# Optimization experiments

Hardware: AMD Instinct MI355X
Metric: run time of the kernel (lower is better)

## Reference

```python
import jax, jax.numpy as jnp
import numpy as np

WS, WS2, UP = 8, 16, 2
DIM, HEADS = 192, 6
HD = DIM // HEADS
SCALE = HD ** -0.5
EPS = 1e-5

def _rel_index():
    r1, c1 = np.meshgrid(np.arange(WS), np.arange(WS), indexing='ij')
    r2, c2 = np.meshgrid(np.arange(WS2), np.arange(WS2), indexing='ij')
    r1, c1 = r1.ravel(), c1.ravel()          # 64 query positions
    r2, c2 = r2.ravel(), c2.ravel()          # 256 kv positions
    rel_row = r1[:, None] - r2[None, :]
    rel_col = c1[:, None] - c2[None, :]
    off = WS * UP - 1    # 15
    span = WS + WS * UP - 1  # 23
    return jnp.asarray((rel_row + off) * span + (rel_col + off))  # (64, 256)

REL_IDX = _rel_index()

def layer_norm(x, w, b):
    m = x.mean(-1, keepdims=True)
    v = ((x - m) ** 2).mean(-1, keepdims=True)
    return (x - m) * jax.lax.rsqrt(v + EPS) * w + b

def window_partition(x, ws):
    B, H, W, C = x.shape
    x = x.reshape(B, H // ws, ws, W // ws, ws, C).transpose(0, 1, 3, 2, 4, 5)
    return x.reshape(-1, ws * ws, C)

def window_reverse(w, ws, H, W, B):
    x = w.reshape(B, H // ws, W // ws, ws, ws, -1).transpose(0, 1, 3, 2, 4, 5)
    return x.reshape(B, H, W, -1)

def setup_inputs() -> dict:
    key = jax.random.key(0)
    ks = jax.random.split(key, 8)
    B, H, W, H2, W2 = 4, 128, 128, 256, 256
    s = 0.02
    return {
        'x': jax.random.normal(ks[0], (B, H * W, DIM), jnp.float32),
        'x2': jax.random.normal(ks[1], (B, H2 * W2, DIM), jnp.float32),
        'norm1_w': jnp.ones((DIM,), jnp.float32),
        'norm1_b': jnp.zeros((DIM,), jnp.float32),
        'qkv_w': jax.random.normal(ks[2], (DIM, DIM), jnp.float32) * s,
        'qkv_b': jnp.zeros((DIM,), jnp.float32),
        'qkv2_w': jax.random.normal(ks[3], (2 * DIM, DIM), jnp.float32) * s,
        'qkv2_b': jnp.zeros((2 * DIM,), jnp.float32),
        'rel_bias': jax.random.normal(ks[4], (23 * 23, HEADS), jnp.float32) * s,
        'proj_w': jax.random.normal(ks[5], (DIM, DIM), jnp.float32) * s,
        'proj_b': jnp.zeros((DIM,), jnp.float32),
        'norm2_w': jnp.ones((DIM,), jnp.float32),
        'norm2_b': jnp.zeros((DIM,), jnp.float32),
        'fc1_w': jax.random.normal(ks[6], (4 * DIM, DIM), jnp.float32) * s,
        'fc1_b': jnp.zeros((4 * DIM,), jnp.float32),
        'fc2_w': jax.random.normal(ks[7], (DIM, 4 * DIM), jnp.float32) * s,
        'fc2_b': jnp.zeros((DIM,), jnp.float32),
        'H': 128, 'W': 128, 'H2': 256, 'W2': 256,
    }

def reference(x, x2, norm1_w, norm1_b, qkv_w, qkv_b, qkv2_w, qkv2_b, rel_bias,
              proj_w, proj_b, norm2_w, norm2_b, fc1_w, fc1_b, fc2_w, fc2_b,
              H, W, H2, W2):
    B, L, C = x.shape
    shortcut = x
    xn = layer_norm(x, norm1_w, norm1_b).reshape(B, H, W, C)
    x2r = x2.reshape(B, H2, W2, C)

    xw = window_partition(xn, WS)      # (nW, 64, C)
    x2w = window_partition(x2r, WS2)   # (nW, 256, C)

    q = (xw @ qkv_w.T + qkv_b).reshape(-1, WS * WS, HEADS, HD).transpose(0, 2, 1, 3)
    kv = (x2w @ qkv2_w.T + qkv2_b).reshape(-1, WS2 * WS2, 2, HEADS, HD).transpose(2, 0, 3, 1, 4)
    k, v = kv[0], kv[1]                # (nW, h, 256, d)

    attn = jnp.einsum('whnd,whmd->whnm', q * SCALE, k)   # (nW, h, 64, 256)
    bias = rel_bias[REL_IDX]                             # (64, 256, h)
    attn = attn + bias.transpose(2, 0, 1)[None]
    attn = jax.nn.softmax(attn, axis=-1)
    out = jnp.einsum('whnm,whmd->wnhd', attn, v).reshape(-1, WS * WS, C)
    out = out @ proj_w.T + proj_b

    x = shortcut + window_reverse(out, WS, H, W, B).reshape(B, H * W, C)
    h = layer_norm(x, norm2_w, norm2_b)
    h = jax.nn.gelu(h @ fc1_w.T + fc1_b, approximate=False)
    x = x + (h @ fc2_w.T + fc2_b)
    return x
```

## Files before the change

### kernel.cpp

```cpp
#include <hip/hip_runtime.h>
#include <hip/hip_bf16.h>
#include <math.h>

typedef unsigned int u32;
typedef unsigned short u16;

typedef __attribute__((ext_vector_type(8))) short bf16x8;
typedef __attribute__((ext_vector_type(4))) float f32x4;

__device__ __forceinline__ float bflo(u32 u){ union{u32 i; float f;} c; c.i = u << 16; return c.f; }
__device__ __forceinline__ float bfhi(u32 u){ union{u32 i; float f;} c; c.i = u & 0xffff0000u; return c.f; }
__device__ __forceinline__ float bfs(u16 s){ union{u32 i; float f;} c; c.i = ((u32)s) << 16; return c.f; }
__device__ __forceinline__ u32 packbf(float a, float b){
  union{float f; u32 i;} ca, cb; ca.f = a; cb.f = b;
  u32 ua = (ca.i + 0x7fffu + ((ca.i >> 16) & 1u)) >> 16;
  u32 ub = (cb.i + 0x7fffu + ((cb.i >> 16) & 1u)) >> 16;
  return (ua & 0xffffu) | (ub << 16);
}
__device__ __forceinline__ u16 bf1(float a){
  union{float f; u32 i;} c; c.f = a;
  return (u16)((c.i + 0x7fffu + ((c.i >> 16) & 1u)) >> 16);
}
__device__ __forceinline__ bf16x8 pack8(float f0,float f1,float f2,float f3,
                                        float f4,float f5,float f6,float f7){
  union { u32 u[4]; bf16x8 v; } cv;
  cv.u[0]=packbf(f0,f1); cv.u[1]=packbf(f2,f3); cv.u[2]=packbf(f4,f5); cv.u[3]=packbf(f6,f7);
  return cv.v;
}
__device__ __forceinline__ float gelu_exact(float v){ return 0.5f*v*(1.0f + erff(v*0.70710678118654752f)); }
__device__ __forceinline__ bool detect_f32(const u32* rawn1){ return (rawn1[0] & 0xFFFFu) == 0u; }

#define SCALE_Q 0.17677669529663687f

#define P_N1W 0
#define P_N1B 192
#define P_N2W 384
#define P_N2B 576
#define P_QKVB 768
#define P_QKV2B 960
#define P_PROJB 1344
#define P_FC1B 1536
#define P_FC2B 2304
#define P_RELB 2496
#define P_TOTAL 5670
#define W_QKV 0
#define W_QKV2 18432
#define W_PROJ 55296
#define W_FC1 73728
#define W_FC2 147456
#define W_TOTAL 221184

__device__ __forceinline__ void stage_w64x192(const u32* __restrict__ src, u32* lds, int tid){
  #pragma unroll
  for (int t = 0; t < 6; ++t) {
    int idx = tid + t*256;
    int j = idx / 24, seg = idx % 24;
    uint4 v = *(const uint4*)(src + (size_t)j*96 + seg*4);
    int byt = (j*384 + seg*16) ^ ((j&7)<<4);
    *(uint4*)((char*)lds + byt) = v;
  }
}
__device__ __forceinline__ bf16x8 lds_w64(const u32* lds, int j, int kt, int g){
  int byt = (j*384 + kt*64 + g*16) ^ ((j&7)<<4);
  return *(const bf16x8*)((const char*)lds + byt);
}
__device__ __forceinline__ bf16x8 lds_w192(const u32* lds, int j, int kk, int g){
  int byt = (j*128 + kk*64 + g*16) ^ ((j&7)<<4);
  return *(const bf16x8*)((const char*)lds + byt);
}

typedef __attribute__((address_space(1))) const u32 gas_u32c;
typedef __attribute__((address_space(3))) u32 las_u32;
__device__ __forceinline__ void gld_lds16(const u32* g, u32* l){
  gas_u32c* gp = (gas_u32c*)(unsigned long long)(size_t)g;
  las_u32*  lp = (las_u32*)(unsigned int)(size_t)l;
  __builtin_amdgcn_global_load_lds(gp, lp, 16, 0, 0);
}
__device__ __forceinline__ void issue_w64x192(const u32* src, u32* lds, int w, int l){
  #pragma unroll
  for (int t = 0; t < 3; ++t) {
    int seg = w + t*8;
    int a = seg*1024 + l*16;
    int j = a / 384;
    int off = a - j*384;
    const u32* g = src + (size_t)j*96 + ((off ^ ((j&7)<<4)) >> 2);
    gld_lds16(g, lds + seg*256);
  }
}
__device__ __forceinline__ void issue_w32x192_t256(const u32* src, u32* lds, int w, int l){
  #pragma unroll
  for (int t = 0; t < 3; ++t) {
    int seg = w + t*4;
    int a = seg*1024 + l*16;
    int j = a / 384;
    int off = a - j*384;
    const u32* g = src + (size_t)j*96 + ((off ^ ((j&7)<<4)) >> 2);
    gld_lds16(g, lds + seg*256);
  }
}
__device__ __forceinline__ void issue_w192x64(const u32* src, int ch, u32* lds, int w, int l){
  #pragma unroll
  for (int t = 0; t < 3; ++t) {
    int seg = w + t*8;
    int a = seg*1024 + l*16;
    int j = a >> 7;
    int off = a & 127;
    const u32* g = src + (size_t)j*384 + ch*32 + ((off ^ ((j&7)<<4)) >> 2);
    gld_lds16(g, lds + seg*256);
  }
}

__global__ __launch_bounds__(256) void k_canon_w(
    const void* qkvw, const void* qkv2w, const void* projw,
    const void* fc1w, const void* fc2w, const u32* rawn1, u32* cw)
{
  int idx = blockIdx.x*256 + threadIdx.x;
  bool isf32 = detect_f32(rawn1);
  const void* src; int off;
  if      (idx < W_QKV2){ src=qkvw;  off=idx; }
  else if (idx < W_PROJ){ src=qkv2w; off=idx-W_QKV2; }
  else if (idx < W_FC1) { src=projw; off=idx-W_PROJ; }
  else if (idx < W_FC2) { src=fc1w;  off=idx-W_FC1; }
  else                  { src=fc2w;  off=idx-W_FC2; }
  u32 o;
  if (isf32) { float2 v = ((const float2*)src)[off]; o = packbf(v.x, v.y); }
  else       { o = ((const u32*)src)[off]; }
  cw[idx] = o;
}

__global__ __launch_bounds__(256) void k_canon_v(
    const void* n1w, const void* n1b, const void* n2w, const void* n2b,
    const void* qkvb, const void* qkv2b, const void* projb,
    const void* fc1b, const void* fc2b, const void* relb,
    const u32* rawn1, float* par)
{
  int idx = blockIdx.x*256 + threadIdx.x;
  if (idx >= P_TOTAL) return;
  bool isf32 = detect_f32(rawn1);
  const void* src; int off;
  if      (idx < P_N1B)  { src=n1w;  off=idx; }
  else if (idx < P_N2W)  { src=n1b;  off=idx-P_N1B; }
  else if (idx < P_N2B)  { src=n2w;  off=idx-P_N2W; }
  else if (idx < P_QKVB) { src=n2b;  off=idx-P_N2B; }
  else if (idx < P_QKV2B){ src=qkvb; off=idx-P_QKVB; }
  else if (idx < P_PROJB){ src=qkv2b;off=idx-P_QKV2B; }
  else if (idx < P_FC1B) { src=projb;off=idx-P_PROJB; }
  else if (idx < P_FC2B) { src=fc1b; off=idx-P_FC1B; }
  else if (idx < P_RELB) { src=fc2b; off=idx-P_FC2B; }
  else                   { src=relb; off=idx-P_RELB; }
  par[idx] = isf32 ? ((const float*)src)[off] : bfs(((const u16*)src)[off]);
}

__global__ __launch_bounds__(256) void k_bias(
    const float* __restrict__ par, float* __restrict__ tbl)
{
  int idx = blockIdx.x*256 + threadIdx.x;
  int h  = idx >> 12;
  int remi = idx & 4095;
  int kt = remi >> 8;
  int qt = (remi >> 6) & 3;
  int ll = idx & 63;
  int lr = ll & 15, g = ll >> 4;
  int q = qt*16 + lr;
  int r1 = q >> 3, c1 = q & 7;
  float vv[4];
  #pragma unroll
  for (int i = 0; i < 4; ++i) {
    int kv = kt*16 + 4*g + i;
    int r2 = kv >> 4, c2 = kv & 15;
    vv[i] = par[P_RELB + ((r1-r2+15)*23 + (c1-c2+15))*6 + h];
  }
  ((float4*)tbl)[idx] = make_float4(vv[0], vv[1], vv[2], vv[3]);
}

__global__ __launch_bounds__(256) void k_qproj(
    const void* __restrict__ x, const u32* __restrict__ rawn1,
    const u32* __restrict__ cw, const float* __restrict__ par,
    u16* __restrict__ q_ws)
{
  __shared__ u32 wbuf[6144];
  int tid = threadIdx.x;
  int l = tid & 63, w = tid >> 6, lr = l & 15, g = l >> 4;
  int wi = blockIdx.x;
  int b = wi >> 8, rem = wi & 255, wh = rem >> 4, ww = rem & 15;
  bool isf32 = detect_f32(rawn1);

  bf16x8 a[6];
  {
    int t = w*16 + lr;
    int r = t >> 3, c = t & 7;
    size_t grow = (size_t)b*16384 + (size_t)(wh*8+r)*128 + (ww*8+c);
    float4 xf[12];
    if (isf32) {
      const float* xp = (const float*)x + grow*192;
      #pragma unroll
      for (int kt = 0; kt < 6; ++kt) {
        xf[kt*2]   = *(const float4*)(xp + kt*32 + 8*g);
        xf[kt*2+1] = *(const float4*)(xp + kt*32 + 8*g + 4);
      }
    } else {
      const u32* xp = (const u32*)x + grow*96;
      #pragma unroll
      for (int kt = 0; kt < 6; ++kt) {
        uint4 u = *(const uint4*)(xp + kt*16 + 4*g);
        xf[kt*2]   = make_float4(bflo(u.x), bfhi(u.x), bflo(u.y), bfhi(u.y));
        xf[kt*2+1] = make_float4(bflo(u.z), bfhi(u.z), bflo(u.w), bfhi(u.w));
      }
    }
    float s = 0.f, s2 = 0.f;
    #pragma unroll
    for (int q8 = 0; q8 < 12; ++q8) {
      s  += xf[q8].x + xf[q8].y + xf[q8].z + xf[q8].w;
      s2 += xf[q8].x*xf[q8].x + xf[q8].y*xf[q8].y + xf[q8].z*xf[q8].z + xf[q8].w*xf[q8].w;
    }
    s += __shfl_xor(s, 16); s2 += __shfl_xor(s2, 16);
    s += __shfl_xor(s, 32); s2 += __shfl_xor(s2, 32);
    float m = s * (1.f/192.f);
    float rstd = rsqrtf(s2*(1.f/192.f) - m*m + 1e-5f);
    #pragma unroll
    for (int kt = 0; kt < 6; ++kt) {
      int k0 = kt*32 + 8*g;
      float4 w0 = *(const float4*)(par + P_N1W + k0);
      float4 w1 = *(const float4*)(par + P_N1W + k0 + 4);
      float4 b0 = *(const float4*)(par + P_N1B + k0);
      float4 b1 = *(const float4*)(par + P_N1B + k0 + 4);
      float4 f0 = xf[kt*2], f1 = xf[kt*2+1];
      a[kt] = pack8((f0.x-m)*rstd*w0.x + b0.x, (f0.y-m)*rstd*w0.y + b0.y,
                    (f0.z-m)*rstd*w0.z + b0.z, (f0.w-m)*rstd*w0.w + b0.w,
                    (f1.x-m)*rstd*w1.x + b1.x, (f1.y-m)*rstd*w1.y + b1.y,
                    (f1.z-m)*rstd*w1.z + b1.z, (f1.w-m)*rstd*w1.w + b1.w);
    }
  }

  for (int ch = 0; ch < 3; ++ch) {
    __syncthreads();
    stage_w64x192(cw + W_QKV + (size_t)(ch*64)*96, wbuf, tid);
    __syncthreads();
    #pragma unroll
    for (int nt2 = 0; nt2 < 4; ++nt2) {
      int j = ch*64 + nt2*16 + lr;
      f32x4 acc = {0.f,0.f,0.f,0.f};
      #pragma unroll
      for (int kt = 0; kt < 6; ++kt) {
        bf16x8 bb = lds_w64(wbuf, nt2*16 + lr, kt, g);
        acc = __builtin_amdgcn_mfma_f32_16x16x32_bf16(a[kt], bb, acc, 0, 0, 0);
      }
      float bj = par[P_QKVB + j];
      int h = j >> 5, d = j & 31;
      #pragma unroll
      for (int i = 0; i < 4; ++i) {
        int n = w*16 + 4*g + i;
        q_ws[(size_t)(wi*6+h)*2048 + (size_t)n*32 + d] = bf1((acc[i] + bj) * SCALE_Q);
      }
    }
  }
}

__global__ __launch_bounds__(256) void k_kvproj(
    const void* __restrict__ x2, const u32* __restrict__ rawn1,
    const u32* __restrict__ cw, const float* __restrict__ par,
    u16* __restrict__ k_ws, u16* __restrict__ v_ws, int win0)
{
  __shared__ u32 wbufA[3072];
  __shared__ u32 wbufB[3072];
  __shared__ u16 otile[64][72];
  int tid = threadIdx.x;
  int l = tid & 63, w = tid >> 6, lr = l & 15, g = l >> 4;
  int lwi = blockIdx.x >> 2, sub = blockIdx.x & 3;
  int wi = win0 + lwi;
  int b = wi >> 8, rem = wi & 255, wh = rem >> 4, ww = rem & 15;
  bool isf32 = detect_f32(rawn1);

  issue_w32x192_t256(cw + W_QKV2, wbufA, w, l);

  bf16x8 a[6];
  {
    int tt = sub*64 + w*16 + lr;
    int r = tt >> 4, c = tt & 15;
    size_t grow = (size_t)b*65536 + (size_t)(wh*16+r)*256 + (ww*16+c);
    if (isf32) {
      const float4* xp = (const float4*)x2 + grow*48;
      #pragma unroll
      for (int kt = 0; kt < 6; ++kt) {
        float4 f0 = xp[kt*8 + g*2];
        float4 f1 = xp[kt*8 + g*2 + 1];
        a[kt] = pack8(f0.x,f0.y,f0.z,f0.w, f1.x,f1.y,f1.z,f1.w);
      }
    } else {
      const u32* xp = (const u32*)x2 + grow*96;
      #pragma unroll
      for (int kt = 0; kt < 6; ++kt)
        a[kt] = *(const bf16x8*)(xp + kt*16 + g*4);
    }
  }
  __syncthreads();

  for (int c = 0; c < 12; ++c) {
    const u32* buf = (c & 1) ? wbufB : wbufA;
    u32* nxt = (c & 1) ? wbufA : wbufB;
    if (c < 11)
      issue_w32x192_t256(cw + W_QKV2 + (size_t)((c+1)*32)*96, nxt, w, l);
    if (c < 6) {
      #pragma unroll
      for (int nt2 = 0; nt2 < 2; ++nt2) {
        int jl = nt2*16 + lr;
        f32x4 acc = {0.f,0.f,0.f,0.f};
        #pragma unroll
        for (int kt = 0; kt < 6; ++kt) {
          bf16x8 bb = lds_w64(buf, jl, kt, g);
          acc = __builtin_amdgcn_mfma_f32_16x16x32_bf16(a[kt], bb, acc, 0, 0, 0);
        }
        float bj = par[P_QKV2B + c*32 + jl];
        #pragma unroll
        for (int i = 0; i < 4; ++i)
          otile[w*16 + 4*g + i][jl] = bf1(acc[i] + bj);
      }
      __syncthreads();
      {
        int tok = tid >> 2, dseg = tid & 3;
        uint4 v = *(const uint4*)&otile[tok][dseg*8];
        *(uint4*)(k_ws + (size_t)(lwi*6 + c)*8192
                        + (size_t)(sub*64 + tok)*32 + dseg*8) = v;
      }
    } else {
      int nv = c - 6;
      #pragma unroll
      for (int nt2 = 0; nt2 < 2; ++nt2) {
        f32x4 acc = {0.f,0.f,0.f,0.f};
        #pragma unroll
        for (int kt = 0; kt < 6; ++kt) {
          bf16x8 bb = lds_w64(buf, nt2*16 + lr, kt, g);
          acc = __builtin_amdgcn_mfma_f32_16x16x32_bf16(bb, a[kt], acc, 0, 0, 0);
        }
        int jl0 = nt2*16 + 4*g;
        #pragma unroll
        for (int i = 0; i < 4; ++i)
          otile[jl0 + i][w*16 + lr] = bf1(acc[i] + par[P_QKV2B + 192 + nv*32 + jl0 + i]);
      }
      __syncthreads();
      {
        int jrow = tid >> 3, seg = tid & 7;
        uint4 v = *(const uint4*)&otile[jrow][seg*8];
        *(uint4*)(v_ws + (size_t)(lwi*6 + nv)*8192 + (size_t)jrow*256
                        + sub*64 + seg*8) = v;
      }
    }
    __syncthreads();
  }
}

__global__ __launch_bounds__(256) void k_attn(
    const u16* __restrict__ q_ws, const u16* __restrict__ k_ws,
    const u16* __restrict__ v_ws, const float* __restrict__ tbl,
    u16* __restrict__ O_ws, int win0)
{
  __shared__ u32 Psh[4*1024];
  __shared__ float msh[2][2][4];
  int tid = threadIdx.x;
  int w = tid >> 6, l = tid & 63;
  int lr = l & 15, g = l >> 4;
  int pairi = w >> 1, half = w & 1;
  int task = blockIdx.x*2 + pairi;
  int lwi = task / 6, h = task - lwi*6;
  int wi = win0 + lwi;

  bf16x8 qb[4];
  {
    const u16* qp = q_ws + (size_t)(wi*6+h)*2048;
    #pragma unroll
    for (int qt = 0; qt < 4; ++qt)
      qb[qt] = *(const bf16x8*)(qp + (qt*16 + lr)*32 + 8*g);
  }
  const u16* kp = k_ws + (size_t)(lwi*6+h)*8192;
  const u16* vp = v_ws + (size_t)(lwi*6+h)*8192;
  const float4* tb4 = (const float4*)tbl + (size_t)h*4096 + l;

  f32x4 ao[2][4];
  #pragma unroll
  for (int dt = 0; dt < 2; ++dt)
    #pragma unroll
    for (int qt = 0; qt < 4; ++qt) ao[dt][qt] = (f32x4){0.f,0.f,0.f,0.f};
  float mreg[4] = {-3.0e38f,-3.0e38f,-3.0e38f,-3.0e38f};
  float sreg[4] = {0.f,0.f,0.f,0.f};
  u32* pbu = Psh + w*1024;

  for (int ch = half*4; ch < half*4 + 4; ++ch) {
    bf16x8 ka0 = *(const bf16x8*)(kp + (2*ch)*512   + lr*32 + 8*g);
    bf16x8 ka1 = *(const bf16x8*)(kp + (2*ch+1)*512 + lr*32 + 8*g);
    f32x4 s0[4], s1[4];
    #pragma unroll
    for (int qt = 0; qt < 4; ++qt) {
      float4 b0 = tb4[(2*ch)*256   + qt*64];
      float4 b1 = tb4[(2*ch+1)*256 + qt*64];
      f32x4 c0; c0[0]=b0.x; c0[1]=b0.y; c0[2]=b0.z; c0[3]=b0.w;
      f32x4 c1; c1[0]=b1.x; c1[1]=b1.y; c1[2]=b1.z; c1[3]=b1.w;
      s0[qt] = __builtin_amdgcn_mfma_f32_16x16x32_bf16(ka0, qb[qt], c0, 0, 0, 0);
      s1[qt] = __builtin_amdgcn_mfma_f32_16x16x32_bf16(ka1, qb[qt], c1, 0, 0, 0);
    }
    #pragma unroll
    for (int qt = 0; qt < 4; ++qt) {
      float pm = fmaxf(fmaxf(fmaxf(s0[qt][0],s0[qt][1]), fmaxf(s0[qt][2],s0[qt][3])),
                       fmaxf(fmaxf(s1[qt][0],s1[qt][1]), fmaxf(s1[qt][2],s1[qt][3])));
      pm = fmaxf(pm, __shfl_xor(pm, 16));
      pm = fmaxf(pm, __shfl_xor(pm, 32));
      if (!__all(pm - mreg[qt] <= 8.0f)) {
        float nm = fmaxf(mreg[qt], pm);
        float resc = __expf(mreg[qt] - nm);
        mreg[qt] = nm;
        sreg[qt] *= resc;
        #pragma unroll
        for (int dt = 0; dt < 2; ++dt) {
          ao[dt][qt][0] *= resc; ao[dt][qt][1] *= resc;
          ao[dt][qt][2] *= resc; ao[dt][qt][3] *= resc;
        }
      }
      float nm = mreg[qt];
      float p00 = __expf(s0[qt][0]-nm), p01 = __expf(s0[qt][1]-nm),
            p02 = __expf(s0[qt][2]-nm), p03 = __expf(s0[qt][3]-nm);
      float p10 = __expf(s1[qt][0]-nm), p11 = __expf(s1[qt][1]-nm),
            p12 = __expf(s1[qt][2]-nm), p13 = __expf(s1[qt][3]-nm);
      float ps = ((p00+p01)+(p02+p03)) + ((p10+p11)+(p12+p13));
      ps += __shfl_xor(ps, 16);
      ps += __shfl_xor(ps, 32);
      sreg[qt] += ps;
      int row = qt*16 + lr;
      int sw = (row & 3) << 2;
      *(uint2*)&pbu[row*16 + ((2*g) ^ sw)]     = make_uint2(packbf(p00,p01), packbf(p02,p03));
      *(uint2*)&pbu[row*16 + ((8 + 2*g) ^ sw)] = make_uint2(packbf(p10,p11), packbf(p12,p13));
    }
    asm volatile("" ::: "memory");
    bf16x8 va0 = *(const bf16x8*)(vp + lr*256        + ch*32 + 8*g);
    bf16x8 va1 = *(const bf16x8*)(vp + (16 + lr)*256 + ch*32 + 8*g);
    #pragma unroll
    for (int qt = 0; qt < 4; ++qt) {
      int row = qt*16 + lr;
      int sw = (row & 3) << 2;
      bf16x8 pa = *(const bf16x8*)&pbu[row*16 + ((4*g) ^ sw)];
      ao[0][qt] = __builtin_amdgcn_mfma_f32_16x16x32_bf16(va0, pa, ao[0][qt], 0, 0, 0);
      ao[1][qt] = __builtin_amdgcn_mfma_f32_16x16x32_bf16(va1, pa, ao[1][qt], 0, 0, 0);
    }
    asm volatile("" ::: "memory");
  }

  __syncthreads();
  if (half == 1) {
    float* dst = (float*)(Psh + pairi*2048);
    #pragma unroll
    for (int dt = 0; dt < 2; ++dt)
      #pragma unroll
      for (int qt = 0; qt < 4; ++qt)
        #pragma unroll
        for (int i = 0; i < 4; ++i)
          dst[(dt*16 + qt*4 + i)*64 + l] = ao[dt][qt][i];
    if (l == 0) {
      msh[pairi][0][0] = mreg[0]; msh[pairi][0][1] = mreg[1];
      msh[pairi][0][2] = mreg[2]; msh[pairi][0][3] = mreg[3];
      msh[pairi][1][0] = sreg[0]; msh[pairi][1][1] = sreg[1];
      msh[pairi][1][2] = sreg[2]; msh[pairi][1][3] = sreg[3];
    }
  }
  __syncthreads();
  if (half == 0) {
    const float* src = (const float*)(Psh + pairi*2048);
    #pragma unroll
    for (int qt = 0; qt < 4; ++qt) {
      float m1 = msh[pairi][0][qt], s1 = msh[pairi][1][qt];
      float M = fmaxf(mreg[qt], m1);
      float e0 = __expf(mreg[qt] - M), e1 = __expf(m1 - M);
      float rs = 1.0f / (sreg[qt]*e0 + s1*e1);
      u16* orow = O_ws + ((size_t)(wi*64) + qt*16 + lr)*192 + h*32;
      #pragma unroll
      for (int dt = 0; dt < 2; ++dt)
        #pragma unroll
        for (int i = 0; i < 4; ++i) {
          float o = ao[dt][qt][i]*e0 + src[(dt*16 + qt*4 + i)*64 + l]*e1;
          orow[dt*16 + 4*g + i] = bf1(o * rs);
        }
    }
  }
}

__global__ __launch_bounds__(256) void k_proj(
    const u16* __restrict__ O_ws, const u32* __restrict__ cw,
    const float* __restrict__ par, const void* __restrict__ x,
    const u32* __restrict__ rawn1, float* __restrict__ xres)
{
  __shared__ u32 wbuf[6144];
  int wi = blockIdx.x;
  int b = wi >> 8, rem = wi & 255, wh = rem >> 4, ww = rem & 15;
  int tid = threadIdx.x;
  int l = tid & 63, w = tid >> 6, lr = l & 15, g = l >> 4;
  bool isf32 = detect_f32(rawn1);
  int t = w*16 + lr;
  const u16* op = O_ws + (size_t)(wi*64 + t)*192;
  bf16x8 a[6];
  #pragma unroll
  for (int kt = 0; kt < 6; ++kt) a[kt] = *(const bf16x8*)(op + kt*32 + 8*g);

  for (int ch = 0; ch < 3; ++ch) {
    __syncthreads();
    stage_w64x192(cw + W_PROJ + (size_t)(ch*64)*96, wbuf, tid);
    __syncthreads();
    #pragma unroll
    for (int nt2 = 0; nt2 < 4; ++nt2) {
      int j = ch*64 + nt2*16 + lr;
      f32x4 acc = {0.f,0.f,0.f,0.f};
      #pragma unroll
      for (int kt = 0; kt < 6; ++kt) {
        bf16x8 bb = lds_w64(wbuf, nt2*16 + lr, kt, g);
        acc = __builtin_amdgcn_mfma_f32_16x16x32_bf16(a[kt], bb, acc, 0, 0, 0);
      }
      float bj = par[P_PROJB + j];
      #pragma unroll
      for (int i = 0; i < 4; ++i) {
        int tok = w*16 + 4*g + i;
        int rr = tok >> 3, cc = tok & 7;
        size_t grow = (size_t)b*16384 + (size_t)(wh*8+rr)*128 + (ww*8+cc);
        float sres = isf32 ? ((const float*)x)[grow*192 + j]
                           : bfs(((const u16*)x)[grow*192 + j]);
        xres[grow*192 + j] = sres + acc[i] + bj;
      }
    }
  }
}

__global__ __launch_bounds__(512) void k_mlp(
    const float* __restrict__ xres, const u32* __restrict__ cw,
    const float* __restrict__ par, float* __restrict__ out)
{
  __shared__ u32 wbufA[6144];
  __shared__ u32 wbufB[6144];
  __shared__ u16 Hc[8][32][64];
  int tid = threadIdx.x;
  int l = tid & 63, w = tid >> 6;
  int lr = l & 15, g = l >> 4;
  size_t row0 = (size_t)blockIdx.x * 256;

  bf16x8 a[2][6];
  #pragma unroll
  for (int mt = 0; mt < 2; ++mt) {
    size_t t = row0 + w*32 + mt*16 + lr;
    const float* xr = xres + t*192;
    float4 xf[12];
    #pragma unroll
    for (int kt = 0; kt < 6; ++kt) {
      xf[kt*2]   = *(const float4*)(xr + kt*32 + 8*g);
      xf[kt*2+1] = *(const float4*)(xr + kt*32 + 8*g + 4);
    }
    float s = 0.f, s2 = 0.f;
    #pragma unroll
    for (int q = 0; q < 12; ++q) {
      s  += xf[q].x + xf[q].y + xf[q].z + xf[q].w;
      s2 += xf[q].x*xf[q].x + xf[q].y*xf[q].y + xf[q].z*xf[q].z + xf[q].w*xf[q].w;
    }
    s += __shfl_xor(s, 16); s2 += __shfl_xor(s2, 16);
    s += __shfl_xor(s, 32); s2 += __shfl_xor(s2, 32);
    float m = s * (1.f/192.f);
    float rstd = rsqrtf(s2*(1.f/192.f) - m*m + 1e-5f);
    #pragma unroll
    for (int kt = 0; kt < 6; ++kt) {
      int k0 = kt*32 + 8*g;
      float4 w0 = *(const float4*)(par + P_N2W + k0);
      float4 w1 = *(const float4*)(par + P_N2W + k0 + 4);
      float4 b0 = *(const float4*)(par + P_N2B + k0);
      float4 b1 = *(const float4*)(par + P_N2B + k0 + 4);
      float4 f0 = xf[kt*2], f1 = xf[kt*2+1];
      a[mt][kt] = pack8((f0.x-m)*rstd*w0.x + b0.x, (f0.y-m)*rstd*w0.y + b0.y,
                        (f0.z-m)*rstd*w0.z + b0.z, (f0.w-m)*rstd*w0.w + b0.w,
                        (f1.x-m)*rstd*w1.x + b1.x, (f1.y-m)*rstd*w1.y + b1.y,
                        (f1.z-m)*rstd*w1.z + b1.z, (f1.w-m)*rstd*w1.w + b1.w);
    }
  }

  f32x4 acc2[2][12];
  #pragma unroll
  for (int mt = 0; mt < 2; ++mt)
    #pragma unroll
    for (int i = 0; i < 12; ++i) acc2[mt][i] = (f32x4){0.f,0.f,0.f,0.f};

  char* hbase = (char*)&Hc[w][0][0];
  const u32* w1p = cw + W_FC1;
  const u32* w2p = cw + W_FC2;

  issue_w64x192(w1p, wbufA, w, l);
  __syncthreads();

  for (int ch = 0; ch < 12; ++ch) {
    issue_w192x64(w2p, ch, wbufB, w, l);
    #pragma unroll
    for (int nt2 = 0; nt2 < 4; ++nt2) {
      f32x4 acc0 = {0.f,0.f,0.f,0.f}, acc1 = {0.f,0.f,0.f,0.f};
      #pragma unroll
      for (int kt = 0; kt < 6; ++kt) {
        bf16x8 bb = lds_w64(wbufA, nt2*16 + lr, kt, g);
        acc0 = __builtin_amdgcn_mfma_f32_16x16x32_bf16(a[0][kt], bb, acc0, 0, 0, 0);
        acc1 = __builtin_amdgcn_mfma_f32_16x16x32_bf16(a[1][kt], bb, acc1, 0, 0, 0);
      }
      float bj = par[P_FC1B + ch*64 + nt2*16 + lr];
      #pragma unroll
      for (int mt = 0; mt < 2; ++mt) {
        f32x4 acc = mt ? acc1 : acc0;
        #pragma unroll
        for (int i = 0; i < 4; ++i) {
          int row = mt*16 + 4*g + i;
          int byt = (row*128 + (nt2*16+lr)*2) ^ ((row&7)<<4);
          *(u16*)(hbase + byt) = bf1(gelu_exact(acc[i] + bj));
        }
      }
    }
    __syncthreads();
    if (ch < 11) issue_w64x192(w1p + (size_t)((ch+1)*64)*96, wbufA, w, l);
    #pragma unroll
    for (int kk = 0; kk < 2; ++kk) {
      bf16x8 a20, a21;
      {
        int row0h = lr, row1h = 16 + lr;
        a20 = *(const bf16x8*)(hbase + ((row0h*128 + kk*64 + g*16) ^ ((row0h&7)<<4)));
        a21 = *(const bf16x8*)(hbase + ((row1h*128 + kk*64 + g*16) ^ ((row1h&7)<<4)));
      }
      #pragma unroll
      for (int nt = 0; nt < 12; ++nt) {
        bf16x8 bb = lds_w192(wbufB, nt*16 + lr, kk, g);
        acc2[0][nt] = __builtin_amdgcn_mfma_f32_16x16x32_bf16(a20, bb, acc2[0][nt], 0, 0, 0);
        acc2[1][nt] = __builtin_amdgcn_mfma_f32_16x16x32_bf16(a21, bb, acc2[1][nt], 0, 0, 0);
      }
    }
    __syncthreads();
  }

  #pragma unroll
  for (int mt = 0; mt < 2; ++mt) {
    size_t trow = row0 + w*32 + mt*16 + 4*g;
    #pragma unroll
    for (int nt = 0; nt < 12; ++nt) {
      int j = nt*16 + lr;
      float bj = par[P_FC2B + j];
      #pragma unroll
      for (int i = 0; i < 4; ++i)
        out[(trow+i)*192 + j] = xres[(trow+i)*192 + j] + acc2[mt][nt][i] + bj;
    }
  }
}

extern "C" void kernel_launch(void* const* d_in, const int* in_sizes, int n_in,
                              void* d_out, int out_size, void* d_ws, size_t ws_size,
                              hipStream_t stream) {
  const void* x      = d_in[0];
  const void* x2     = d_in[1];
  const void* n1w    = d_in[2];
  const void* n1b    = d_in[3];
  const void* qkv_w  = d_in[4];
  const void* qkv_b  = d_in[5];
  const void* qkv2_w = d_in[6];
  const void* qkv2_b = d_in[7];
  const void* relb   = d_in[8];
  const void* proj_w = d_in[9];
  const void* proj_b = d_in[10];
  const void* n2w    = d_in[11];
  const void* n2b    = d_in[12];
  const void* fc1_w  = d_in[13];
  const void* fc1_b  = d_in[14];
  const void* fc2_w  = d_in[15];
  const void* fc2_b  = d_in[16];
  const u32* rawn1   = (const u32*)d_in[2];
  float* out = (float*)d_out;

  int nslice = (ws_size >= 303290520ull) ? 1 : (ws_size >= 202700000ull) ? 2 : 4;
  int nw = 1024 / nslice;
  size_t kvb = (size_t)nw * 98304;

  char* ws = (char*)d_ws;
  u16*   q_ws = (u16*)ws;
  u16*   k_ws = (u16*)(ws + 25165824);
  u16*   v_ws = (u16*)(ws + 25165824 + kvb);
  u16*   O_ws = (u16*)(ws + 25165824 + 2*kvb);
  float* xres = (float*)(ws + 50331648 + 2*kvb);
  u32*   cw   = (u32*)(ws + 100663296 + 2*kvb);
  float* tbl  = (float*)(ws + 100663296 + 2*kvb + 884736);
  float* par  = (float*)(ws + 100663296 + 2*kvb + 884736 + 393216);

  k_canon_w<<<W_TOTAL/256, 256, 0, stream>>>(qkv_w, qkv2_w, proj_w, fc1_w, fc2_w, rawn1, cw);
  k_canon_v<<<(P_TOTAL+255)/256, 256, 0, stream>>>(n1w, n1b, n2w, n2b, qkv_b, qkv2_b,
                                                   proj_b, fc1_b, fc2_b, relb, rawn1, par);
  k_bias  <<<96, 256, 0, stream>>>(par, tbl);
  k_qproj <<<1024, 256, 0, stream>>>(x, rawn1, cw, par, q_ws);
  for (int s = 0; s < nslice; ++s) {
    int win0 = s*nw;
    k_kvproj<<<nw*4, 256, 0, stream>>>(x2, rawn1, cw, par, k_ws, v_ws, win0);
    k_attn  <<<nw*3, 256, 0, stream>>>(q_ws, k_ws, v_ws, tbl, O_ws, win0);
  }
  k_proj  <<<1024, 256, 0, stream>>>(O_ws, cw, par, x, rawn1, xres);
  k_mlp   <<< 256, 512, 0, stream>>>(xres, cw, par, out);
}
```

Measured before the change: 630.8 us.

## Process a whole KV window per 512-thread block in kvproj

The KV projection kernel now handles all 256 tokens of a window in one 512-thread block, with each wave computing two 16-row M tiles, instead of four 256-thread blocks each taking 64 tokens. Each streamed weight chunk in LDS is then reused across four times as many rows, which cuts the weight traffic from global memory into LDS by that factor. The output staging tile grows to cover the full window, so V rows are stored as whole 256-wide contiguous rows. The cost is more LDS and registers per block and fewer blocks, which may lower occupancy and latency hiding.

```diff
diff --git a/kernel.cpp b/kernel.cpp
--- a/kernel.cpp
+++ b/kernel.cpp
@@ -87,10 +87,17 @@
     gld_lds16(g, lds + seg*256);
   }
 }
-__device__ __forceinline__ void issue_w32x192_t256(const u32* src, u32* lds, int w, int l){
-  #pragma unroll
-  for (int t = 0; t < 3; ++t) {
-    int seg = w + t*4;
+__device__ __forceinline__ void issue_w32x192_t512(const u32* src, u32* lds, int w, int l){
+  {
+    int seg = w;
+    int a = seg*1024 + l*16;
+    int j = a / 384;
+    int off = a - j*384;
+    const u32* g = src + (size_t)j*96 + ((off ^ ((j&7)<<4)) >> 2);
+    gld_lds16(g, lds + seg*256);
+  }
+  if (w < 4) {
+    int seg = w + 8;
     int a = seg*1024 + l*16;
     int j = a / 384;
     int off = a - j*384;
@@ -256,26 +263,27 @@
   }
 }
 
-__global__ __launch_bounds__(256) void k_kvproj(
+__global__ __launch_bounds__(512) void k_kvproj(
     const void* __restrict__ x2, const u32* __restrict__ rawn1,
     const u32* __restrict__ cw, const float* __restrict__ par,
     u16* __restrict__ k_ws, u16* __restrict__ v_ws, int win0)
 {
   __shared__ u32 wbufA[3072];
   __shared__ u32 wbufB[3072];
-  __shared__ u16 otile[64][72];
+  __shared__ u16 ot[12288];
   int tid = threadIdx.x;
   int l = tid & 63, w = tid >> 6, lr = l & 15, g = l >> 4;
-  int lwi = blockIdx.x >> 2, sub = blockIdx.x & 3;
+  int lwi = blockIdx.x;
   int wi = win0 + lwi;
   int b = wi >> 8, rem = wi & 255, wh = rem >> 4, ww = rem & 15;
   bool isf32 = detect_f32(rawn1);
 
-  issue_w32x192_t256(cw + W_QKV2, wbufA, w, l);
-
-  bf16x8 a[6];
-  {
-    int tt = sub*64 + w*16 + lr;
+  issue_w32x192_t512(cw + W_QKV2, wbufA, w, l);
+
+  bf16x8 a[2][6];
+  #pragma unroll
+  for (int mt = 0; mt < 2; ++mt) {
+    int tt = w*32 + mt*16 + lr;
     int r = tt >> 4, c = tt & 15;
     size_t grow = (size_t)b*65536 + (size_t)(wh*16+r)*256 + (ww*16+c);
     if (isf32) {
@@ -284,13 +292,13 @@
       for (int kt = 0; kt < 6; ++kt) {
         float4 f0 = xp[kt*8 + g*2];
         float4 f1 = xp[kt*8 + g*2 + 1];
-        a[kt] = pack8(f0.x,f0.y,f0.z,f0.w, f1.x,f1.y,f1.z,f1.w);
+        a[mt][kt] = pack8(f0.x,f0.y,f0.z,f0.w, f1.x,f1.y,f1.z,f1.w);
       }
     } else {
       const u32* xp = (const u32*)x2 + grow*96;
       #pragma unroll
       for (int kt = 0; kt < 6; ++kt)
-        a[kt] = *(const bf16x8*)(xp + kt*16 + g*4);
+        a[mt][kt] = *(const bf16x8*)(xp + kt*16 + g*4);
     }
   }
   __syncthreads();
@@ -299,50 +307,56 @@
     const u32* buf = (c & 1) ? wbufB : wbufA;
     u32* nxt = (c & 1) ? wbufA : wbufB;
     if (c < 11)
-      issue_w32x192_t256(cw + W_QKV2 + (size_t)((c+1)*32)*96, nxt, w, l);
+      issue_w32x192_t512(cw + W_QKV2 + (size_t)((c+1)*32)*96, nxt, w, l);
     if (c < 6) {
       #pragma unroll
-      for (int nt2 = 0; nt2 < 2; ++nt2) {
-        int jl = nt2*16 + lr;
-        f32x4 acc = {0.f,0.f,0.f,0.f};
+      for (int mt = 0; mt < 2; ++mt)
         #pragma unroll
-        for (int kt = 0; kt < 6; ++kt) {
-          bf16x8 bb = lds_w64(buf, jl, kt, g);
-          acc = __builtin_amdgcn_mfma_f32_16x16x32_bf16(a[kt], bb, acc, 0, 0, 0);
+        for (int nt2 = 0; nt2 < 2; ++nt2) {
+          int jl = nt2*16 + lr;
+          f32x4 acc = {0.f,0.f,0.f,0.f};
+          #pragma unroll
+          for (int kt = 0; kt < 6; ++kt) {
+            bf16x8 bb = lds_w64(buf, jl, kt, g);
+            acc = __builtin_amdgcn_mfma_f32_16x16x32_bf16(a[mt][kt], bb, acc, 0, 0, 0);
+          }
+          float bj = par[P_QKV2B + c*32 + jl];
+          #pragma unroll
+          for (int i = 0; i < 4; ++i)
+            ot[(w*32 + mt*16 + 4*g + i)*48 + jl] = bf1(acc[i] + bj);
         }
-        float bj = par[P_QKV2B + c*32 + jl];
-        #pragma unroll
-        for (int i = 0; i < 4; ++i)
-          otile[w*16 + 4*g + i][jl] = bf1(acc[i] + bj);
-      }
       __syncthreads();
-      {
-        int tok = tid >> 2, dseg = tid & 3;
-        uint4 v = *(const uint4*)&otile[tok][dseg*8];
-        *(uint4*)(k_ws + (size_t)(lwi*6 + c)*8192
-                        + (size_t)(sub*64 + tok)*32 + dseg*8) = v;
+      #pragma unroll
+      for (int t = 0; t < 2; ++t) {
+        int u = tid + t*512;
+        int tok = u >> 2, dseg = u & 3;
+        uint4 v = *(const uint4*)&ot[tok*48 + dseg*8];
+        *(uint4*)(k_ws + (size_t)(lwi*6 + c)*8192 + (size_t)tok*32 + dseg*8) = v;
       }
     } else {
       int nv = c - 6;
       #pragma unroll
-      for (int nt2 = 0; nt2 < 2; ++nt2) {
-        f32x4 acc = {0.f,0.f,0.f,0.f};
+      for (int mt = 0; mt < 2; ++mt)
         #pragma unroll
-        for (int kt = 0; kt < 6; ++kt) {
-          bf16x8 bb = lds_w64(buf, nt2*16 + lr, kt, g);
-          acc = __builtin_amdgcn_mfma_f32_16x16x32_bf16(bb, a[kt], acc, 0, 0, 0);
+        for (int nt2 = 0; nt2 < 2; ++nt2) {
+          f32x4 acc = {0.f,0.f,0.f,0.f};
+          #pragma unroll
+          for (int kt = 0; kt < 6; ++kt) {
+            bf16x8 bb = lds_w64(buf, nt2*16 + lr, kt, g);
+            acc = __builtin_amdgcn_mfma_f32_16x16x32_bf16(bb, a[mt][kt], acc, 0, 0, 0);
+          }
+          int jl0 = nt2*16 + 4*g;
+          #pragma unroll
+          for (int i = 0; i < 4; ++i)
+            ot[(jl0 + i)*264 + w*32 + mt*16 + lr] = bf1(acc[i] + par[P_QKV2B + 192 + nv*32 + jl0 + i]);
         }
-        int jl0 = nt2*16 + 4*g;
-        #pragma unroll
-        for (int i = 0; i < 4; ++i)
-          otile[jl0 + i][w*16 + lr] = bf1(acc[i] + par[P_QKV2B + 192 + nv*32 + jl0 + i]);
-      }
       __syncthreads();
-      {
-        int jrow = tid >> 3, seg = tid & 7;
-        uint4 v = *(const uint4*)&otile[jrow][seg*8];
-        *(uint4*)(v_ws + (size_t)(lwi*6 + nv)*8192 + (size_t)jrow*256
-                        + sub*64 + seg*8) = v;
+      #pragma unroll
+      for (int t = 0; t < 2; ++t) {
+        int u = tid + t*512;
+        int jrow = u >> 5, seg = u & 31;
+        uint4 v = *(const uint4*)&ot[jrow*264 + seg*8];
+        *(uint4*)(v_ws + (size_t)(lwi*6 + nv)*8192 + (size_t)jrow*256 + seg*8) = v;
       }
     }
     __syncthreads();
@@ -686,7 +700,7 @@
   k_qproj <<<1024, 256, 0, stream>>>(x, rawn1, cw, par, q_ws);
   for (int s = 0; s < nslice; ++s) {
     int win0 = s*nw;
-    k_kvproj<<<nw*4, 256, 0, stream>>>(x2, rawn1, cw, par, k_ws, v_ws, win0);
+    k_kvproj<<<nw,   512, 0, stream>>>(x2, rawn1, cw, par, k_ws, v_ws, win0);
     k_attn  <<<nw*3, 256, 0, stream>>>(q_ws, k_ws, v_ws, tbl, O_ws, win0);
   }
   k_proj  <<<1024, 256, 0, stream>>>(O_ws, cw, par, x, rawn1, xres);
```

After: 631.5 us. No clear change (+0.1%).
